# Kernel tuning notes

Measured on AMD Instinct MI355X. Metric: run time of the kernel, lower is better.

The kernel has to match this reference:

```python
import jax, jax.numpy as jnp
import numpy as np

B, T, D = 2, 2048, 1024
H = 16
HD = D // H
NE = 17  # n_edge_types + 1

def setup_inputs() -> dict:
    key = jax.random.key(0)
    ks = jax.random.split(key, 6)
    x = jax.random.normal(ks[0], (B, T, D), dtype=jnp.float32)
    graph_adj = jax.random.uniform(ks[1], (B, T, T), dtype=jnp.float32)
    edge_types = jax.random.randint(ks[2], (B, T, T), 0, NE, dtype=jnp.int32)
    Wqkv = jax.random.normal(ks[3], (D, 3 * D), dtype=jnp.float32) * (D ** -0.5)
    Wproj = jax.random.normal(ks[4], (D, D), dtype=jnp.float32) * (D ** -0.5)
    adj_bias = jnp.zeros((H,), dtype=jnp.float32)
    edge_table = jax.random.normal(ks[5], (NE, H), dtype=jnp.float32) * 0.02
    return {"x": x, "graph_adj": graph_adj, "edge_types": edge_types,
            "Wqkv": Wqkv, "Wproj": Wproj, "adj_bias": adj_bias,
            "edge_table": edge_table}

def reference(x, graph_adj, edge_types, Wqkv, Wproj, adj_bias, edge_table):
    Bc, Tc, C = x.shape
    qkv = (x @ Wqkv).reshape(Bc, Tc, 3, H, HD)
    q, k, v = qkv[:, :, 0], qkv[:, :, 1], qkv[:, :, 2]  # [B,T,H,HD]
    scale = 1.0 / jnp.sqrt(jnp.asarray(HD, dtype=x.dtype))
    # scores: [B,H,T,T]
    attn = jnp.einsum('bqhd,bkhd->bhqk', q, k) * scale
    # adjacency bias per head
    attn = attn + adj_bias[None, :, None, None] * graph_adj[:, None, :, :]
    # edge-type bias: lookup [B,T,T,H] -> [B,H,T,T]
    etype_b = edge_table[edge_types]  # [B,T,T,H]
    attn = attn + jnp.transpose(etype_b, (0, 3, 1, 2))
    # causal mask (upper triangle, diag=1)
    causal = jnp.triu(jnp.ones((Tc, Tc), dtype=bool), k=1)
    attn = jnp.where(causal[None, None, :, :], jnp.asarray(-jnp.inf, dtype=attn.dtype), attn)
    attn = jax.nn.softmax(attn, axis=-1)
    out = jnp.einsum('bhqk,bkhd->bqhd', attn, v).reshape(Bc, Tc, C)
    return out @ Wproj
```

## Files before the change

### kernel.cpp

```cpp
#include <hip/hip_runtime.h>
#include <stdint.h>

#define TT 2048
#define HH 16
#define LOG2E 1.44269504089f

typedef _Float16 f16;
typedef __attribute__((ext_vector_type(8))) _Float16 f16x8;
typedef __attribute__((ext_vector_type(4))) _Float16 f16x4;
typedef __attribute__((ext_vector_type(4))) float f32x4;
typedef unsigned short ushort_t;

__device__ __forceinline__ void gl_lds16(const void* g, void* l){
  __builtin_amdgcn_global_load_lds(
      (__attribute__((address_space(1))) void*)(void*)g,
      (__attribute__((address_space(3))) void*)l, 16, 0, 0);
}

__device__ __forceinline__ void lds_barrier(){
  __asm__ volatile("s_waitcnt lgkmcnt(0)\n\ts_barrier" ::: "memory");
}

struct SchedT { unsigned short v[80]; };
static constexpr SchedT make_sched(){
  SchedT s{};
  int idx = 0;
  for (int size = 8; size >= 1; --size){
    for (int qt = 31; qt >= 8; --qt){
      int full = qt >> 3;
      int tail = (qt & 7) + 1;
      if (size == 8)
        for (int ci = 0; ci < full; ++ci)
          s.v[idx++] = (unsigned short)(qt | (ci << 8));
      if (tail == size)
        s.v[idx++] = (unsigned short)(qt | (full << 8));
    }
    s.v[idx++] = (unsigned short)(size - 1);
  }
  return s;
}
__constant__ SchedT SCHED = make_sched();

__device__ __forceinline__ int slot_base(int qt){
  return (qt < 16) ? 2 * (qt - 8)
       : (qt < 24) ? 16 + 3 * (qt - 16)
                   : 40 + 4 * (qt - 24);
}

__global__ __launch_bounds__(256) void cvt_f2h_kernel(const float4* __restrict__ in,
                                                      uint2* __restrict__ out, int n4){
  int i = blockIdx.x * 256 + threadIdx.x;
  if (i >= n4) return;
  float4 v = in[i];
  union { f16 h[4]; uint2 u; } o;
  o.h[0] = (f16)v.x; o.h[1] = (f16)v.y; o.h[2] = (f16)v.z; o.h[3] = (f16)v.w;
  out[i] = o.u;
}

__global__ __launch_bounds__(256) void pack_bias_kernel(const float* __restrict__ gadj,
                                                        const int* __restrict__ etype,
                                                        uint32_t* __restrict__ out){
  int bid = blockIdx.x;
  int b = bid / 528, ti = bid - b * 528;
  int qt = (int)((sqrtf(8.f * (float)ti + 1.f) - 1.f) * 0.5f);
  while ((qt + 1) * (qt + 2) / 2 <= ti) ++qt;
  while (qt * (qt + 1) / 2 > ti) --qt;
  int kt = ti - qt * (qt + 1) / 2;

  int t = threadIdx.x;
  int row = t >> 2, c0 = (t & 3) << 4;
  size_t src = ((size_t)b * TT + qt * 64 + row) * TT + kt * 64 + c0;
  uint32_t* dst = out + (size_t)bid * 4096;
  int wq = (row >> 4) * 64 + (row & 15);
  #pragma unroll
  for (int v4 = 0; v4 < 4; ++v4){
    float4 g = *(const float4*)(gadj + src + v4 * 4);
    int4   e = *(const int4*)(etype + src + v4 * 4);
    union { f16 h; ushort_t u; } c;
    uint4 o;
    c.h = (f16)g.x; o.x = (uint32_t)c.u | ((uint32_t)e.x << 16);
    c.h = (f16)g.y; o.y = (uint32_t)c.u | ((uint32_t)e.y << 16);
    c.h = (f16)g.z; o.z = (uint32_t)c.u | ((uint32_t)e.z << 16);
    c.h = (f16)g.w; o.w = (uint32_t)c.u | ((uint32_t)e.w << 16);
    *(uint4*)(dst + (((size_t)(wq + v4 * 16)) << 4) + ((t & 3) << 2)) = o;
  }
}

__global__ __launch_bounds__(256) void transpose_cvt_kernel(const float* __restrict__ in,
                                                            f16* __restrict__ out, int R, int C){
  __shared__ float tile[64][65];
  int c0 = blockIdx.x * 64, r0 = blockIdx.y * 64;
  int t = threadIdx.x;
  int row = t >> 2, cs = (t & 3) << 4;
  const float4* src = (const float4*)(in + (size_t)(r0 + row) * C + c0 + cs);
  float4 a = src[0], b = src[1], c = src[2], d = src[3];
  float* tr = &tile[row][cs];
  tr[0]=a.x; tr[1]=a.y; tr[2]=a.z;  tr[3]=a.w;
  tr[4]=b.x; tr[5]=b.y; tr[6]=b.z;  tr[7]=b.w;
  tr[8]=c.x; tr[9]=c.y; tr[10]=c.z; tr[11]=c.w;
  tr[12]=d.x;tr[13]=d.y;tr[14]=d.z; tr[15]=d.w;
  __syncthreads();
  f16 tmp[16];
  #pragma unroll
  for (int j = 0; j < 16; ++j) tmp[j] = (f16)tile[cs + j][row];
  f16* dst = out + (size_t)(c0 + row) * R + r0 + cs;
  *(uint4*)dst = *(uint4*)&tmp[0];
  *(uint4*)(dst + 8) = *(uint4*)&tmp[8];
}

template<int BN>
__global__ __launch_bounds__(256) void gemm_f16_kernel(const f16* __restrict__ A,
                                                       const f16* __restrict__ Bt,
                                                       void* __restrict__ Cout,
                                                       int M, int N, int K, int out_f32){
  constexpr int WN = BN / 2;
  constexpr int NI = WN / 16;
  __shared__ __align__(16) f16 As[128 * 32];
  __shared__ __align__(16) f16 Bs[BN * 32];
  int t = threadIdx.x;
  int w = t >> 6, lane = t & 63;
  int wm = (w >> 1) * 64, wn = (w & 1) * WN;
  int lrow = lane & 15, quad = lane >> 4;
  int bm = blockIdx.y, bn = blockIdx.x;

  f32x4 acc[4][NI];
  for (int i = 0; i < 4; ++i)
    for (int j = 0; j < NI; ++j)
      for (int r = 0; r < 4; ++r) acc[i][j][r] = 0.f;

  const int nk = K >> 5;
  for (int kt = 0; kt < nk; ++kt){
    int k0 = kt << 5;
    __syncthreads();
    #pragma unroll
    for (int i = 0; i < 2; ++i){
      int c = (w << 7) + (i << 6) + lane;
      gl_lds16(A + (size_t)((bm << 7) + (c >> 2)) * K + k0 + ((c & 3) << 3),
               As + ((w << 7) + (i << 6)) * 8);
      if constexpr (BN == 128){
        gl_lds16(Bt + (size_t)((bn << 7) + (c >> 2)) * K + k0 + ((c & 3) << 3),
                 Bs + ((w << 7) + (i << 6)) * 8);
      }
    }
    if constexpr (BN == 64){
      int c = (w << 6) + lane;
      gl_lds16(Bt + (size_t)((bn << 6) + (c >> 2)) * K + k0 + ((c & 3) << 3),
               Bs + (w << 6) * 8);
    }
    __syncthreads();
    f16x8 af[4], bfr[NI];
    #pragma unroll
    for (int mi = 0; mi < 4; ++mi)
      af[mi] = *(const f16x8*)(As + (wm + mi * 16 + lrow) * 32 + quad * 8);
    #pragma unroll
    for (int ni = 0; ni < NI; ++ni)
      bfr[ni] = *(const f16x8*)(Bs + (wn + ni * 16 + lrow) * 32 + quad * 8);
    #pragma unroll
    for (int mi = 0; mi < 4; ++mi)
      #pragma unroll
      for (int ni = 0; ni < NI; ++ni)
        acc[mi][ni] = __builtin_amdgcn_mfma_f32_16x16x32_f16(af[mi], bfr[ni], acc[mi][ni], 0, 0, 0);
  }

  #pragma unroll
  for (int mi = 0; mi < 4; ++mi)
    #pragma unroll
    for (int ni = 0; ni < NI; ++ni)
      #pragma unroll
      for (int r = 0; r < 4; ++r){
        int row = (bm << 7) + wm + mi * 16 + quad * 4 + r;
        int col = bn * BN + wn + ni * 16 + lrow;
        float val = acc[mi][ni][r];
        if (out_f32) ((float*)Cout)[(size_t)row * N + col] = val;
        else         ((f16*)Cout)[(size_t)row * N + col] = (f16)val;
      }
}

__global__ __launch_bounds__(256, 4) void attn_kernel(const f16* __restrict__ qkv,
                                                      const uint32_t* __restrict__ pbias,
                                                      const float* __restrict__ adj_bias,
                                                      const float* __restrict__ edge_table,
                                                      f16* __restrict__ attn_out,
                                                      f16* __restrict__ Opart,
                                                      float* __restrict__ MLpart){
  __shared__ __align__(16) f16 Ks[64 * 72];
  __shared__ __align__(16) f16 Vt[64 * 72];
  __shared__ float edge_lds[32 * 17];

  int bx = blockIdx.x;
  int bh = bx & 31;
  int h = bh & 15, b = bh >> 4;
  int ej = SCHED.v[bx >> 5];
  int qt = ej & 31, ci = ej >> 8;
  int ksrt = ci << 3;
  int kend = min(qt, ksrt + 7);
  bool whole = (qt < 8);

  int t = threadIdx.x;
  int w = t >> 6, lane = t & 63;
  int lrow = lane & 15, quad = lane >> 4;

  for (int i = t; i < 544; i += 256)
    edge_lds[i] = edge_table[(i % 17) * HH + h] * LOG2E;
  float adjb = adj_bias[h] * LOG2E;
  int erep = (lane & 31) * 17;

  int q0 = qt * 64 + w * 16;
  const size_t qrow = ((size_t)b * TT + q0 + lrow) * 3072 + h * 64;
  f16x8 qf0 = *(const f16x8*)(qkv + qrow + quad * 8);
  f16x8 qf1 = *(const f16x8*)(qkv + qrow + 32 + quad * 8);

  f32x4 o[4];
  for (int i = 0; i < 4; ++i)
    for (int r = 0; r < 4; ++r) o[i][r] = 0.f;
  float mrun = -1e30f, lrun = 0.f;

  const int keyA = (t >> 3) << 1;
  const int hdA  = (t & 7) << 3;
  const int sA   = ((keyA >> 3) ^ (hdA >> 3)) & 7;
  const f16* kbase = qkv + (size_t)b * TT * 3072 + 1024 + h * 64;
  const f16* vbase = qkv + (size_t)b * TT * 3072 + 2048 + h * 64;
  const size_t koffA = (size_t)keyA * 3072 + hdA;
  const size_t koffB = koffA + 3072;

  const float SCL = 0.125f * LOG2E;

  const int tribase = b * 528 + ((qt * (qt + 1)) >> 1);
  const uint32_t* bthread = pbias + ((size_t)t << 4);
  const int qg = q0 + lrow;

  uint4 ka, kb, va, vb;
  {
    const f16* kr = kbase + (size_t)(ksrt * 64) * 3072;
    const f16* vr = vbase + (size_t)(ksrt * 64) * 3072;
    ka = *(const uint4*)(kr + koffA); kb = *(const uint4*)(kr + koffB);
    va = *(const uint4*)(vr + koffA); vb = *(const uint4*)(vr + koffB);
  }

  for (int kt2 = ksrt; kt2 <= kend; ++kt2){
    lds_barrier();
    union B4 { uint4 v; uint32_t e[4]; } bb0, bb1, bb2, bb3;
    {
      const uint32_t* tp = bthread + ((size_t)(tribase + kt2) << 12);
      bb0.v = *(const uint4*)(tp + 0);
      bb1.v = *(const uint4*)(tp + 4);
      bb2.v = *(const uint4*)(tp + 8);
      bb3.v = *(const uint4*)(tp + 12);
    }
    *(uint4*)(Ks + keyA * 72 + hdA) = ka;
    *(uint4*)(Ks + (keyA + 1) * 72 + hdA) = kb;
    {
      union { uint4 u; f16 hh[8]; } ua, ub;
      ua.u = va; ub.u = vb;
      #pragma unroll
      for (int jj = 0; jj < 8; ++jj){
        union { f16 h[2]; uint32_t wv; } pr;
        pr.h[0] = ua.hh[jj]; pr.h[1] = ub.hh[jj];
        *(uint32_t*)(Vt + (hdA + jj) * 72 + (sA << 3) + (keyA & 7)) = pr.wv;
      }
    }
    if (kt2 < kend){
      const f16* kr = kbase + (size_t)((kt2 + 1) * 64) * 3072;
      const f16* vr = vbase + (size_t)((kt2 + 1) * 64) * 3072;
      ka = *(const uint4*)(kr + koffA); kb = *(const uint4*)(kr + koffB);
      va = *(const uint4*)(vr + koffA); vb = *(const uint4*)(vr + koffB);
    }
    lds_barrier();

    f32x4 sf[4];
    #pragma unroll
    for (int nb = 0; nb < 4; ++nb){
      f32x4 s = {0.f, 0.f, 0.f, 0.f};
      f16x8 kf0 = *(const f16x8*)(Ks + (nb * 16 + lrow) * 72 + quad * 8);
      f16x8 kf1 = *(const f16x8*)(Ks + (nb * 16 + lrow) * 72 + 32 + quad * 8);
      s = __builtin_amdgcn_mfma_f32_16x16x32_f16(kf0, qf0, s, 0, 0, 0);
      s = __builtin_amdgcn_mfma_f32_16x16x32_f16(kf1, qf1, s, 0, 0, 0);
      sf[nb] = s;
    }

    int kq = kt2 * 64 + quad * 4;
    float sarr[4][4];
    bool diag = (kt2 == qt);
#define MASK_NB(nb, BB)                                                          \
    {                                                                            \
      _Pragma("unroll")                                                          \
      for (int r = 0; r < 4; ++r){                                               \
        float v;                                                                 \
        if (diag && (kq + nb * 16 + r > qg)) v = -1e30f;                         \
        else {                                                                   \
          uint32_t bp = BB.e[r];                                                 \
          union { ushort_t u; f16 h; } cv; cv.u = (ushort_t)bp;                  \
          v = sf[nb][r] * SCL + adjb * (float)cv.h + edge_lds[erep + (bp >> 16)];\
        }                                                                        \
        sarr[nb][r] = v;                                                         \
      }                                                                          \
    }
    MASK_NB(0, bb0)
    MASK_NB(1, bb1)
    MASK_NB(2, bb2)
    MASK_NB(3, bb3)
#undef MASK_NB

    float m_ = -1e30f;
    #pragma unroll
    for (int nb = 0; nb < 4; ++nb)
      #pragma unroll
      for (int r = 0; r < 4; ++r)
        m_ = fmaxf(m_, sarr[nb][r]);
    m_ = fmaxf(m_, __shfl_xor(m_, 16));
    m_ = fmaxf(m_, __shfl_xor(m_, 32));
    bool need = (m_ > mrun + 5.0f);
    if (__any(need)){
      float mnew = fmaxf(mrun, m_);
      float alpha = exp2f(mrun - mnew);
      lrun *= alpha;
      #pragma unroll
      for (int r = 0; r < 4; ++r){
        float ar = __shfl(alpha, (quad << 2) | r);
        #pragma unroll
        for (int nbh = 0; nbh < 4; ++nbh) o[nbh][r] *= ar;
      }
      mrun = mnew;
    }
    float rs = 0.f;
    #pragma unroll
    for (int nb = 0; nb < 4; ++nb)
      #pragma unroll
      for (int r = 0; r < 4; ++r){
        float p = exp2f(sarr[nb][r] - mrun);
        sarr[nb][r] = p; rs += p;
      }
    rs += __shfl_xor(rs, 16);
    rs += __shfl_xor(rs, 32);
    lrun += rs;

    f16x4 pa[4];
    #pragma unroll
    for (int nb = 0; nb < 4; ++nb){
      pa[nb][0] = (f16)sarr[nb][0];
      pa[nb][1] = (f16)sarr[nb][1];
      pa[nb][2] = (f16)sarr[nb][2];
      pa[nb][3] = (f16)sarr[nb][3];
    }

    #pragma unroll
    for (int nb = 0; nb < 4; ++nb){
      #pragma unroll
      for (int nbh = 0; nbh < 4; ++nbh){
        int hd = nbh * 16 + lrow;
        int s2 = ((nb * 2 + (quad >> 1)) ^ (hd >> 3)) & 7;
        f16x4 vf = *(const f16x4*)(Vt + hd * 72 + (s2 << 3) + ((quad & 1) << 2));
        o[nbh] = __builtin_amdgcn_mfma_f32_16x16x16f16(pa[nb], vf, o[nbh], 0, 0, 0);
      }
    }
  }

  if (whole){
    #pragma unroll
    for (int r = 0; r < 4; ++r){
      float inv = 1.0f / __shfl(lrun, (quad << 2) | r);
      int qg2 = q0 + quad * 4 + r;
      #pragma unroll
      for (int nbh = 0; nbh < 4; ++nbh){
        int col = h * 64 + nbh * 16 + lrow;
        attn_out[((size_t)b * TT + qg2) * 1024 + col] = (f16)(o[nbh][r] * inv);
      }
    }
  } else {
    int slot = bh * 72 + slot_base(qt) + ci;
    f16* Ob = Opart + (size_t)slot * 4096;
    #pragma unroll
    for (int nbh = 0; nbh < 4; ++nbh)
      #pragma unroll
      for (int r = 0; r < 4; ++r)
        Ob[(w * 16 + quad * 4 + r) * 64 + nbh * 16 + lrow] = (f16)o[nbh][r];
    if (quad == 0){
      MLpart[(size_t)slot * 128 + w * 16 + lrow] = mrun;
      MLpart[(size_t)slot * 128 + 64 + w * 16 + lrow] = lrun;
    }
  }
}

__global__ __launch_bounds__(256) void combine_kernel(const f16* __restrict__ Opart,
                                                      const float* __restrict__ ML,
                                                      f16* __restrict__ attn_out){
  int qt = blockIdx.x + 8;
  int bh = blockIdx.y;
  int nch = (qt >> 3) + 1;
  int slot0 = bh * 72 + slot_base(qt);
  int t = threadIdx.x;
  int q = t >> 2;
  int hd0 = (t & 3) << 4;

  float m[4], l[4];
  float M = -1e30f;
  #pragma unroll
  for (int c = 0; c < 4; ++c){
    if (c < nch){
      m[c] = ML[(size_t)(slot0 + c) * 128 + q];
      l[c] = ML[(size_t)(slot0 + c) * 128 + 64 + q];
      M = fmaxf(M, m[c]);
    } else { m[c] = -1e30f; l[c] = 0.f; }
  }
  float acc[16];
  #pragma unroll
  for (int i = 0; i < 16; ++i) acc[i] = 0.f;
  float L = 0.f;
  #pragma unroll
  for (int c = 0; c < 4; ++c){
    if (c < nch){
      float wgt = exp2f(m[c] - M);
      L += l[c] * wgt;
      const f16* O = Opart + (size_t)(slot0 + c) * 4096 + q * 64 + hd0;
      f16x8 a0 = *(const f16x8*)O, a1 = *(const f16x8*)(O + 8);
      #pragma unroll
      for (int i = 0; i < 8; ++i){
        acc[i]     += (float)a0[i] * wgt;
        acc[i + 8] += (float)a1[i] * wgt;
      }
    }
  }
  float invL = 1.0f / L;
  f16 outv[16];
  #pragma unroll
  for (int i = 0; i < 16; ++i) outv[i] = (f16)(acc[i] * invL);
  int b = bh >> 4, h = bh & 15;
  f16* dst = attn_out + ((size_t)b * TT + qt * 64 + q) * 1024 + h * 64 + hd0;
  *(uint4*)dst = *(uint4*)&outv[0];
  *(uint4*)(dst + 8) = *(uint4*)&outv[8];
}

extern "C" void kernel_launch(void* const* d_in, const int* in_sizes, int n_in,
                              void* d_out, int out_size, void* d_ws, size_t ws_size,
                              hipStream_t stream){
  (void)in_sizes; (void)n_in; (void)out_size; (void)ws_size;
  const float* x_f32  = (const float*)d_in[0];
  const float* gadj   = (const float*)d_in[1];
  const int*   etype  = (const int*)d_in[2];
  const float* wqkv   = (const float*)d_in[3];
  const float* wproj  = (const float*)d_in[4];
  const float* adjb   = (const float*)d_in[5];
  const float* etab   = (const float*)d_in[6];

  char* ws = (char*)d_ws;
  f16*     x_f16  = (f16*)(ws);
  f16*     qkv    = (f16*)(ws + (8u  << 20));
  f16*     wqkvT  = (f16*)(ws + (32u << 20));
  f16*     Opart  = (f16*)(ws + (32u << 20));
  f16*     wprojT = (f16*)(ws + (51u << 20));
  float*   MLpart = (float*)(ws + (53u << 20));
  uint32_t* pbias = (uint32_t*)(ws + (55u << 20));
  f16*     attn_o = x_f16;

  cvt_f2h_kernel<<<4096, 256, 0, stream>>>((const float4*)x_f32, (uint2*)x_f16, 1048576);
  pack_bias_kernel<<<1056, 256, 0, stream>>>(gadj, etype, pbias);
  transpose_cvt_kernel<<<dim3(48, 16), 256, 0, stream>>>(wqkv, wqkvT, 1024, 3072);
  transpose_cvt_kernel<<<dim3(16, 16), 256, 0, stream>>>(wproj, wprojT, 1024, 1024);
  gemm_f16_kernel<128><<<dim3(24, 32), 256, 0, stream>>>(x_f16, wqkvT, qkv, 4096, 3072, 1024, 0);
  attn_kernel<<<2560, 256, 0, stream>>>(qkv, pbias, adjb, etab, attn_o, Opart, MLpart);
  combine_kernel<<<dim3(24, 32), 256, 0, stream>>>(Opart, MLpart, attn_o);
  gemm_f16_kernel<64><<<dim3(16, 32), 256, 0, stream>>>(attn_o, wprojT, d_out, 4096, 1024, 1024, 1);
}
```

Measured before the change: 281.9 us.

## Use 128-row query tiles with 512-thread blocks sharing K/V LDS tiles

The attention kernel now handles 128 query rows per block with 8 waves instead of 64 rows with 4 waves, so each K/V tile loaded into LDS is reused by twice as many queries. K and V loading is split by role: half the threads stage V (transposed) and half stage K. The schedule, split-KV slot layout and combine kernel are rebuilt for 128-row tiles. The cost is some idle waves on diagonal tiles where the lower 64-row half is masked, and higher register and LDS pressure per block at 512 threads.

```diff
diff --git a/kernel.cpp b/kernel.cpp
--- a/kernel.cpp
+++ b/kernel.cpp
@@ -21,30 +21,25 @@
   __asm__ volatile("s_waitcnt lgkmcnt(0)\n\ts_barrier" ::: "memory");
 }
 
-struct SchedT { unsigned short v[80]; };
+struct SchedT { unsigned short v[40]; };
 static constexpr SchedT make_sched(){
-  SchedT s{};
-  int idx = 0;
-  for (int size = 8; size >= 1; --size){
-    for (int qt = 31; qt >= 8; --qt){
-      int full = qt >> 3;
-      int tail = (qt & 7) + 1;
+  SchedT s{}; int idx = 0;
+  for (int size = 8; size >= 1; --size)
+    for (int J = 15; J >= 0; --J){
+      int NT = 2 * J + 2;
+      int f = NT >> 3, tail = NT - (f << 3);
       if (size == 8)
-        for (int ci = 0; ci < full; ++ci)
-          s.v[idx++] = (unsigned short)(qt | (ci << 8));
-      if (tail == size)
-        s.v[idx++] = (unsigned short)(qt | (full << 8));
-    }
-    s.v[idx++] = (unsigned short)(size - 1);
-  }
+        for (int ci = 0; ci < f; ++ci) s.v[idx++] = (unsigned short)(J | (ci << 4));
+      if (tail == size) s.v[idx++] = (unsigned short)(J | (f << 4));
+    }
   return s;
 }
 __constant__ SchedT SCHED = make_sched();
 
-__device__ __forceinline__ int slot_base(int qt){
-  return (qt < 16) ? 2 * (qt - 8)
-       : (qt < 24) ? 16 + 3 * (qt - 16)
-                   : 40 + 4 * (qt - 24);
+__device__ __forceinline__ int slot_base(int J){
+  return (J < 8) ? 2 * (J - 4)
+       : (J < 12) ? 8 + 3 * (J - 8)
+                  : 20 + 4 * (J - 12);
 }
 
 __global__ __launch_bounds__(256) void cvt_f2h_kernel(const float4* __restrict__ in,
@@ -176,7 +171,7 @@
       }
 }
 
-__global__ __launch_bounds__(256, 4) void attn_kernel(const f16* __restrict__ qkv,
+__global__ __launch_bounds__(512, 4) void attn_kernel(const f16* __restrict__ qkv,
                                                       const uint32_t* __restrict__ pbias,
                                                       const float* __restrict__ adj_bias,
                                                       const float* __restrict__ edge_table,
@@ -191,21 +186,22 @@
   int bh = bx & 31;
   int h = bh & 15, b = bh >> 4;
   int ej = SCHED.v[bx >> 5];
-  int qt = ej & 31, ci = ej >> 8;
-  int ksrt = ci << 3;
-  int kend = min(qt, ksrt + 7);
-  bool whole = (qt < 8);
+  int J = ej & 15, ci = ej >> 4;
+  int kts = ci << 3;
+  int kend = min(2 * J + 1, kts + 7);
+  bool whole = (J <= 3);
 
   int t = threadIdx.x;
   int w = t >> 6, lane = t & 63;
   int lrow = lane & 15, quad = lane >> 4;
 
-  for (int i = t; i < 544; i += 256)
+  for (int i = t; i < 544; i += 512)
     edge_lds[i] = edge_table[(i % 17) * HH + h] * LOG2E;
   float adjb = adj_bias[h] * LOG2E;
   int erep = (lane & 31) * 17;
 
-  int q0 = qt * 64 + w * 16;
+  const int qt_w = 2 * J + (w >> 2);
+  const int q0 = J * 128 + w * 16;
   const size_t qrow = ((size_t)b * TT + q0 + lrow) * 3072 + h * 64;
   f16x8 qf0 = *(const f16x8*)(qkv + qrow + quad * 8);
   f16x8 qf1 = *(const f16x8*)(qkv + qrow + 32 + quad * 8);
@@ -215,142 +211,156 @@
     for (int r = 0; r < 4; ++r) o[i][r] = 0.f;
   float mrun = -1e30f, lrun = 0.f;
 
-  const int keyA = (t >> 3) << 1;
-  const int hdA  = (t & 7) << 3;
-  const int sA   = ((keyA >> 3) ^ (hdA >> 3)) & 7;
+  const bool vrole = (t < 256);
+  const int vkeyA = (t >> 3) << 1;
+  const int vhd   = (t & 7) << 3;
+  const int vs    = ((vkeyA >> 3) ^ (vhd >> 3)) & 7;
+  const int tt    = t - 256;
+  const int kkey  = tt >> 2;
+  const int khd   = (tt & 3) << 4;
   const f16* kbase = qkv + (size_t)b * TT * 3072 + 1024 + h * 64;
   const f16* vbase = qkv + (size_t)b * TT * 3072 + 2048 + h * 64;
-  const size_t koffA = (size_t)keyA * 3072 + hdA;
-  const size_t koffB = koffA + 3072;
 
   const float SCL = 0.125f * LOG2E;
 
-  const int tribase = b * 528 + ((qt * (qt + 1)) >> 1);
-  const uint32_t* bthread = pbias + ((size_t)t << 4);
+  const int tri_w = b * 528 + ((qt_w * (qt_w + 1)) >> 1);
+  const uint32_t* bthread = pbias + ((size_t)(((w & 3) << 6) | lane) << 4);
   const int qg = q0 + lrow;
 
-  uint4 ka, kb, va, vb;
-  {
-    const f16* kr = kbase + (size_t)(ksrt * 64) * 3072;
-    const f16* vr = vbase + (size_t)(ksrt * 64) * 3072;
-    ka = *(const uint4*)(kr + koffA); kb = *(const uint4*)(kr + koffB);
-    va = *(const uint4*)(vr + koffA); vb = *(const uint4*)(vr + koffB);
-  }
-
-  for (int kt2 = ksrt; kt2 <= kend; ++kt2){
+  uint4 ra, rb;
+  if (vrole){
+    const f16* vr = vbase + (size_t)(kts * 64) * 3072;
+    ra = *(const uint4*)(vr + (size_t)vkeyA * 3072 + vhd);
+    rb = *(const uint4*)(vr + (size_t)(vkeyA + 1) * 3072 + vhd);
+  } else {
+    const f16* kr = kbase + (size_t)(kts * 64) * 3072;
+    ra = *(const uint4*)(kr + (size_t)kkey * 3072 + khd);
+    rb = *(const uint4*)(kr + (size_t)kkey * 3072 + khd + 8);
+  }
+
+  for (int kt2 = kts; kt2 <= kend; ++kt2){
+    bool act = (kt2 <= qt_w);
     lds_barrier();
     union B4 { uint4 v; uint32_t e[4]; } bb0, bb1, bb2, bb3;
-    {
-      const uint32_t* tp = bthread + ((size_t)(tribase + kt2) << 12);
+    if (act){
+      const uint32_t* tp = bthread + ((size_t)(tri_w + kt2) << 12);
       bb0.v = *(const uint4*)(tp + 0);
       bb1.v = *(const uint4*)(tp + 4);
       bb2.v = *(const uint4*)(tp + 8);
       bb3.v = *(const uint4*)(tp + 12);
     }
-    *(uint4*)(Ks + keyA * 72 + hdA) = ka;
-    *(uint4*)(Ks + (keyA + 1) * 72 + hdA) = kb;
-    {
+    if (vrole){
       union { uint4 u; f16 hh[8]; } ua, ub;
-      ua.u = va; ub.u = vb;
+      ua.u = ra; ub.u = rb;
       #pragma unroll
       for (int jj = 0; jj < 8; ++jj){
         union { f16 h[2]; uint32_t wv; } pr;
         pr.h[0] = ua.hh[jj]; pr.h[1] = ub.hh[jj];
-        *(uint32_t*)(Vt + (hdA + jj) * 72 + (sA << 3) + (keyA & 7)) = pr.wv;
-      }
+        *(uint32_t*)(Vt + (vhd + jj) * 72 + (vs << 3) + (vkeyA & 7)) = pr.wv;
+      }
+    } else {
+      *(uint4*)(Ks + kkey * 72 + khd) = ra;
+      *(uint4*)(Ks + kkey * 72 + khd + 8) = rb;
     }
     if (kt2 < kend){
-      const f16* kr = kbase + (size_t)((kt2 + 1) * 64) * 3072;
-      const f16* vr = vbase + (size_t)((kt2 + 1) * 64) * 3072;
-      ka = *(const uint4*)(kr + koffA); kb = *(const uint4*)(kr + koffB);
-      va = *(const uint4*)(vr + koffA); vb = *(const uint4*)(vr + koffB);
+      if (vrole){
+        const f16* vr = vbase + (size_t)((kt2 + 1) * 64) * 3072;
+        ra = *(const uint4*)(vr + (size_t)vkeyA * 3072 + vhd);
+        rb = *(const uint4*)(vr + (size_t)(vkeyA + 1) * 3072 + vhd);
+      } else {
+        const f16* kr = kbase + (size_t)((kt2 + 1) * 64) * 3072;
+        ra = *(const uint4*)(kr + (size_t)kkey * 3072 + khd);
+        rb = *(const uint4*)(kr + (size_t)kkey * 3072 + khd + 8);
+      }
     }
     lds_barrier();
 
-    f32x4 sf[4];
-    #pragma unroll
-    for (int nb = 0; nb < 4; ++nb){
-      f32x4 s = {0.f, 0.f, 0.f, 0.f};
-      f16x8 kf0 = *(const f16x8*)(Ks + (nb * 16 + lrow) * 72 + quad * 8);
-      f16x8 kf1 = *(const f16x8*)(Ks + (nb * 16 + lrow) * 72 + 32 + quad * 8);
-      s = __builtin_amdgcn_mfma_f32_16x16x32_f16(kf0, qf0, s, 0, 0, 0);
-      s = __builtin_amdgcn_mfma_f32_16x16x32_f16(kf1, qf1, s, 0, 0, 0);
-      sf[nb] = s;
-    }
-
-    int kq = kt2 * 64 + quad * 4;
-    float sarr[4][4];
-    bool diag = (kt2 == qt);
+    if (act){
+      f32x4 sf[4];
+      #pragma unroll
+      for (int nb = 0; nb < 4; ++nb){
+        f32x4 s = {0.f, 0.f, 0.f, 0.f};
+        f16x8 kf0 = *(const f16x8*)(Ks + (nb * 16 + lrow) * 72 + quad * 8);
+        f16x8 kf1 = *(const f16x8*)(Ks + (nb * 16 + lrow) * 72 + 32 + quad * 8);
+        s = __builtin_amdgcn_mfma_f32_16x16x32_f16(kf0, qf0, s, 0, 0, 0);
+        s = __builtin_amdgcn_mfma_f32_16x16x32_f16(kf1, qf1, s, 0, 0, 0);
+        sf[nb] = s;
+      }
+
+      int kq = kt2 * 64 + quad * 4;
+      float sarr[4][4];
+      bool diag = (kt2 == qt_w);
 #define MASK_NB(nb, BB)                                                          \
-    {                                                                            \
-      _Pragma("unroll")                                                          \
-      for (int r = 0; r < 4; ++r){                                               \
-        float v;                                                                 \
-        if (diag && (kq + nb * 16 + r > qg)) v = -1e30f;                         \
-        else {                                                                   \
-          uint32_t bp = BB.e[r];                                                 \
-          union { ushort_t u; f16 h; } cv; cv.u = (ushort_t)bp;                  \
-          v = sf[nb][r] * SCL + adjb * (float)cv.h + edge_lds[erep + (bp >> 16)];\
+      {                                                                          \
+        _Pragma("unroll")                                                        \
+        for (int r = 0; r < 4; ++r){                                             \
+          float v;                                                               \
+          if (diag && (kq + nb * 16 + r > qg)) v = -1e30f;                       \
+          else {                                                                 \
+            uint32_t bp = BB.e[r];                                               \
+            union { ushort_t u; f16 h; } cv; cv.u = (ushort_t)bp;                \
+            v = sf[nb][r]*SCL + adjb*(float)cv.h + edge_lds[erep + (bp >> 16)];  \
+          }                                                                      \
+          sarr[nb][r] = v;                                                       \
         }                                                                        \
-        sarr[nb][r] = v;                                                         \
-      }                                                                          \
-    }
-    MASK_NB(0, bb0)
-    MASK_NB(1, bb1)
-    MASK_NB(2, bb2)
-    MASK_NB(3, bb3)
+      }
+      MASK_NB(0, bb0)
+      MASK_NB(1, bb1)
+      MASK_NB(2, bb2)
+      MASK_NB(3, bb3)
 #undef MASK_NB
 
-    float m_ = -1e30f;
-    #pragma unroll
-    for (int nb = 0; nb < 4; ++nb)
-      #pragma unroll
-      for (int r = 0; r < 4; ++r)
-        m_ = fmaxf(m_, sarr[nb][r]);
-    m_ = fmaxf(m_, __shfl_xor(m_, 16));
-    m_ = fmaxf(m_, __shfl_xor(m_, 32));
-    bool need = (m_ > mrun + 5.0f);
-    if (__any(need)){
-      float mnew = fmaxf(mrun, m_);
-      float alpha = exp2f(mrun - mnew);
-      lrun *= alpha;
-      #pragma unroll
-      for (int r = 0; r < 4; ++r){
-        float ar = __shfl(alpha, (quad << 2) | r);
+      float m_ = -1e30f;
+      #pragma unroll
+      for (int nb = 0; nb < 4; ++nb)
         #pragma unroll
-        for (int nbh = 0; nbh < 4; ++nbh) o[nbh][r] *= ar;
-      }
-      mrun = mnew;
-    }
-    float rs = 0.f;
-    #pragma unroll
-    for (int nb = 0; nb < 4; ++nb)
-      #pragma unroll
-      for (int r = 0; r < 4; ++r){
-        float p = exp2f(sarr[nb][r] - mrun);
-        sarr[nb][r] = p; rs += p;
-      }
-    rs += __shfl_xor(rs, 16);
-    rs += __shfl_xor(rs, 32);
-    lrun += rs;
-
-    f16x4 pa[4];
-    #pragma unroll
-    for (int nb = 0; nb < 4; ++nb){
-      pa[nb][0] = (f16)sarr[nb][0];
-      pa[nb][1] = (f16)sarr[nb][1];
-      pa[nb][2] = (f16)sarr[nb][2];
-      pa[nb][3] = (f16)sarr[nb][3];
-    }
-
-    #pragma unroll
-    for (int nb = 0; nb < 4; ++nb){
-      #pragma unroll
-      for (int nbh = 0; nbh < 4; ++nbh){
-        int hd = nbh * 16 + lrow;
-        int s2 = ((nb * 2 + (quad >> 1)) ^ (hd >> 3)) & 7;
-        f16x4 vf = *(const f16x4*)(Vt + hd * 72 + (s2 << 3) + ((quad & 1) << 2));
-        o[nbh] = __builtin_amdgcn_mfma_f32_16x16x16f16(pa[nb], vf, o[nbh], 0, 0, 0);
+        for (int r = 0; r < 4; ++r)
+          m_ = fmaxf(m_, sarr[nb][r]);
+      m_ = fmaxf(m_, __shfl_xor(m_, 16));
+      m_ = fmaxf(m_, __shfl_xor(m_, 32));
+      bool need = (m_ > mrun + 5.0f);
+      if (__any(need)){
+        float mnew = fmaxf(mrun, m_);
+        float alpha = exp2f(mrun - mnew);
+        lrun *= alpha;
+        #pragma unroll
+        for (int r = 0; r < 4; ++r){
+          float ar = __shfl(alpha, (quad << 2) | r);
+          #pragma unroll
+          for (int nbh = 0; nbh < 4; ++nbh) o[nbh][r] *= ar;
+        }
+        mrun = mnew;
+      }
+      float rs = 0.f;
+      #pragma unroll
+      for (int nb = 0; nb < 4; ++nb)
+        #pragma unroll
+        for (int r = 0; r < 4; ++r){
+          float p = exp2f(sarr[nb][r] - mrun);
+          sarr[nb][r] = p; rs += p;
+        }
+      rs += __shfl_xor(rs, 16);
+      rs += __shfl_xor(rs, 32);
+      lrun += rs;
+
+      f16x4 pa[4];
+      #pragma unroll
+      for (int nb = 0; nb < 4; ++nb){
+        pa[nb][0] = (f16)sarr[nb][0];
+        pa[nb][1] = (f16)sarr[nb][1];
+        pa[nb][2] = (f16)sarr[nb][2];
+        pa[nb][3] = (f16)sarr[nb][3];
+      }
+
+      #pragma unroll
+      for (int nb = 0; nb < 4; ++nb){
+        #pragma unroll
+        for (int nbh = 0; nbh < 4; ++nbh){
+          int hd = nbh * 16 + lrow;
+          int s2 = ((nb * 2 + (quad >> 1)) ^ (hd >> 3)) & 7;
+          f16x4 vf = *(const f16x4*)(Vt + hd * 72 + (s2 << 3) + ((quad & 1) << 2));
+          o[nbh] = __builtin_amdgcn_mfma_f32_16x16x16f16(pa[nb], vf, o[nbh], 0, 0, 0);
+        }
       }
     }
   }
@@ -367,16 +377,16 @@
       }
     }
   } else {
-    int slot = bh * 72 + slot_base(qt) + ci;
-    f16* Ob = Opart + (size_t)slot * 4096;
+    int slot = bh * 36 + slot_base(J) + ci;
+    f16* Ob = Opart + (size_t)slot * 8192;
     #pragma unroll
     for (int nbh = 0; nbh < 4; ++nbh)
       #pragma unroll
       for (int r = 0; r < 4; ++r)
         Ob[(w * 16 + quad * 4 + r) * 64 + nbh * 16 + lrow] = (f16)o[nbh][r];
     if (quad == 0){
-      MLpart[(size_t)slot * 128 + w * 16 + lrow] = mrun;
-      MLpart[(size_t)slot * 128 + 64 + w * 16 + lrow] = lrun;
+      MLpart[(size_t)slot * 256 + w * 16 + lrow] = mrun;
+      MLpart[(size_t)slot * 256 + 128 + w * 16 + lrow] = lrun;
     }
   }
 }
@@ -384,50 +394,56 @@
 __global__ __launch_bounds__(256) void combine_kernel(const f16* __restrict__ Opart,
                                                       const float* __restrict__ ML,
                                                       f16* __restrict__ attn_out){
-  int qt = blockIdx.x + 8;
+  int J = blockIdx.x + 4;
   int bh = blockIdx.y;
-  int nch = (qt >> 3) + 1;
-  int slot0 = bh * 72 + slot_base(qt);
+  int nch = (J < 8) ? 2 : ((J < 12) ? 3 : 4);
+  int slot0 = bh * 36 + slot_base(J);
   int t = threadIdx.x;
-  int q = t >> 2;
-  int hd0 = (t & 3) << 4;
+  int row = t >> 1;
+  int hd0 = (t & 1) << 5;
 
   float m[4], l[4];
   float M = -1e30f;
   #pragma unroll
   for (int c = 0; c < 4; ++c){
     if (c < nch){
-      m[c] = ML[(size_t)(slot0 + c) * 128 + q];
-      l[c] = ML[(size_t)(slot0 + c) * 128 + 64 + q];
+      m[c] = ML[(size_t)(slot0 + c) * 256 + row];
+      l[c] = ML[(size_t)(slot0 + c) * 256 + 128 + row];
       M = fmaxf(M, m[c]);
     } else { m[c] = -1e30f; l[c] = 0.f; }
   }
-  float acc[16];
-  #pragma unroll
-  for (int i = 0; i < 16; ++i) acc[i] = 0.f;
+  float acc[32];
+  #pragma unroll
+  for (int i = 0; i < 32; ++i) acc[i] = 0.f;
   float L = 0.f;
   #pragma unroll
   for (int c = 0; c < 4; ++c){
     if (c < nch){
       float wgt = exp2f(m[c] - M);
       L += l[c] * wgt;
-      const f16* O = Opart + (size_t)(slot0 + c) * 4096 + q * 64 + hd0;
-      f16x8 a0 = *(const f16x8*)O, a1 = *(const f16x8*)(O + 8);
+      const f16* O = Opart + (size_t)(slot0 + c) * 8192 + row * 64 + hd0;
+      f16x8 a0 = *(const f16x8*)O,        a1 = *(const f16x8*)(O + 8);
+      f16x8 a2 = *(const f16x8*)(O + 16), a3 = *(const f16x8*)(O + 24);
       #pragma unroll
       for (int i = 0; i < 8; ++i){
-        acc[i]     += (float)a0[i] * wgt;
-        acc[i + 8] += (float)a1[i] * wgt;
+        acc[i]      += (float)a0[i] * wgt;
+        acc[i + 8]  += (float)a1[i] * wgt;
+        acc[i + 16] += (float)a2[i] * wgt;
+        acc[i + 24] += (float)a3[i] * wgt;
       }
     }
   }
   float invL = 1.0f / L;
-  f16 outv[16];
-  #pragma unroll
-  for (int i = 0; i < 16; ++i) outv[i] = (f16)(acc[i] * invL);
+  f16 outv[32];
+  #pragma unroll
+  for (int i = 0; i < 32; ++i) outv[i] = (f16)(acc[i] * invL);
   int b = bh >> 4, h = bh & 15;
-  f16* dst = attn_out + ((size_t)b * TT + qt * 64 + q) * 1024 + h * 64 + hd0;
+  int qg = J * 128 + row;
+  f16* dst = attn_out + ((size_t)b * TT + qg) * 1024 + h * 64 + hd0;
   *(uint4*)dst = *(uint4*)&outv[0];
   *(uint4*)(dst + 8) = *(uint4*)&outv[8];
+  *(uint4*)(dst + 16) = *(uint4*)&outv[16];
+  *(uint4*)(dst + 24) = *(uint4*)&outv[24];
 }
 
 extern "C" void kernel_launch(void* const* d_in, const int* in_sizes, int n_in,
@@ -457,7 +473,7 @@
   transpose_cvt_kernel<<<dim3(48, 16), 256, 0, stream>>>(wqkv, wqkvT, 1024, 3072);
   transpose_cvt_kernel<<<dim3(16, 16), 256, 0, stream>>>(wproj, wprojT, 1024, 1024);
   gemm_f16_kernel<128><<<dim3(24, 32), 256, 0, stream>>>(x_f16, wqkvT, qkv, 4096, 3072, 1024, 0);
-  attn_kernel<<<2560, 256, 0, stream>>>(qkv, pbias, adjb, etab, attn_o, Opart, MLpart);
-  combine_kernel<<<dim3(24, 32), 256, 0, stream>>>(Opart, MLpart, attn_o);
+  attn_kernel<<<1280, 512, 0, stream>>>(qkv, pbias, adjb, etab, attn_o, Opart, MLpart);
+  combine_kernel<<<dim3(12, 32), 256, 0, stream>>>(Opart, MLpart, attn_o);
   gemm_f16_kernel<64><<<dim3(16, 32), 256, 0, stream>>>(attn_o, wprojT, d_out, 4096, 1024, 1024, 1);
 }
```

Result: no change. 281.0 us (-0.3%).
